# Performance work log

Measured on AMD Instinct MI355X. Metric: run time of the kernel, lower is better.

## Reference

```python
import jax, jax.numpy as jnp
import numpy as np
from jax import lax

KSIZE = 7

def _grid():
    # torch.linspace(-7//2, 7//2, 7) == linspace(-4, 3, 7): asymmetric, step 7/6
    x = np.linspace(-4.0, 3.0, KSIZE, dtype=np.float32).reshape(-1, 1)
    y = x.T
    return x, y

def _gaussian_kernel(sigma):
    x, y = _grid()
    g = np.exp(-(x ** 2 + y ** 2) / (2.0 * sigma ** 2))
    g = g / g.sum()
    return g.reshape(1, 1, KSIZE, KSIZE).astype(np.float32)

def _log_kernel(sigma):
    x, y = _grid()
    r2 = x ** 2 + y ** 2
    log = (1.0 - r2 / (2.0 * sigma ** 2)) * np.exp(-r2 / (2.0 * sigma ** 2))
    log = log / np.abs(log).sum()
    return log.reshape(1, 1, KSIZE, KSIZE).astype(np.float32)

SOBEL_X = jnp.asarray([[-1, 0, 1], [-2, 0, 2], [-1, 0, 1]], dtype=jnp.float32).reshape(1, 1, 3, 3)
SOBEL_Y = jnp.asarray([[-1, -2, -1], [0, 0, 0], [1, 2, 1]], dtype=jnp.float32).reshape(1, 1, 3, 3)
POINT = jnp.asarray([[0, -1, 0], [-1, 4, -1], [0, -1, 0]], dtype=jnp.float32).reshape(1, 1, 3, 3)
STRUCT_FILTERS = [jnp.asarray(_gaussian_kernel(s)) for s in (0.5, 1.0, 2.0)]
SCALE_FILTERS = [jnp.asarray(_log_kernel(s)) for s in (1.0, 2.0, 4.0)]

def _conv(x, k, pad):
    # torch F.conv2d == cross-correlation, which lax conv also computes (no kernel flip)
    return lax.conv_general_dilated(
        x, k, window_strides=(1, 1),
        padding=[(pad, pad), (pad, pad)],
        dimension_numbers=("NCHW", "OIHW", "NCHW"))

def _mse(a, b):
    d = a - b
    return jnp.mean(d * d)

def _maxpool3(x):
    # torch max_pool2d pads with -inf
    return lax.reduce_window(
        x, -jnp.inf, lax.max,
        window_dimensions=(1, 1, 3, 3), window_strides=(1, 1, 1, 1),
        padding=[(0, 0), (0, 0), (1, 1), (1, 1)])

def setup_inputs() -> dict:
    key = jax.random.key(0)
    k1, k2 = jax.random.split(key)
    shape = (64, 1, 512, 512)
    return {
        "reconstruction": jax.random.normal(k1, shape, dtype=jnp.float32),
        "target": jax.random.normal(k2, shape, dtype=jnp.float32),
    }

def reference(reconstruction, target):
    # intensity-weighted reconstruction loss
    w = (target > target.mean()).astype(reconstruction.dtype) * 2.0 + 1.0
    recon_loss = _mse(reconstruction * w, target * w)

    # gradient (sobel) loss
    gradient_loss = (
        _mse(_conv(reconstruction, SOBEL_X, 1), _conv(target, SOBEL_X, 1)) +
        _mse(_conv(reconstruction, SOBEL_Y, 1), _conv(target, SOBEL_Y, 1)))

    # point-source (laplacian) loss
    point_loss = _mse(_conv(reconstruction, POINT, 1), _conv(target, POINT, 1))

    # multi-scale gaussian structure loss
    structure_loss = 0.0
    for f in STRUCT_FILTERS:
        structure_loss += _mse(_conv(reconstruction, f, KSIZE // 2), _conv(target, f, KSIZE // 2))

    # LoG blob-scale loss
    scale_loss = 0.0
    for f in SCALE_FILTERS:
        scale_loss += _mse(_conv(reconstruction, f, KSIZE // 2), _conv(target, f, KSIZE // 2))

    # peak preservation via 3x3 max pool + L1
    peak_loss = jnp.mean(jnp.abs(_maxpool3(reconstruction) - _maxpool3(target)))

    return (recon_loss + 2.0 * gradient_loss + 1.5 * point_loss +
            1.0 * structure_loss + 1.0 * scale_loss + 2.0 * peak_loss)
```

## Files before the change

kernel.cpp:

```cpp
#include <hip/hip_runtime.h>
#include <math.h>

#define IMG 512
#define IMG2 (IMG * IMG)
#define NPIX (64 * IMG2)
#define ZPB 16

__device__ float g_c[64];

typedef __fp16 h2_t __attribute__((ext_vector_type(2)));

__device__ __forceinline__ float rdfl(float x) {
    return __uint_as_float(__builtin_amdgcn_readfirstlane(__float_as_uint(x)));
}
__device__ __forceinline__ unsigned int rdflu(float x) {
    return __builtin_amdgcn_readfirstlane(__float_as_uint(x));
}
__device__ __forceinline__ unsigned int as_u(h2_t h) {
    union { h2_t h; unsigned int u; } c;
    c.h = h;
    return c.u;
}
__device__ __forceinline__ h2_t as_h2(unsigned int u) {
    union { unsigned int u; h2_t h; } c;
    c.u = u;
    return c.h;
}
__device__ __forceinline__ h2_t h2z() {
    h2_t z = {(__fp16)0.f, (__fp16)0.f};
    return z;
}

__global__ void precompute_kernel() {
    if (threadIdx.x != 0 || blockIdx.x != 0) return;
    const double step = 7.0 / 6.0;
    float x[7];
    for (int j = 0; j < 7; j++) x[j] = (float)(-4.0 + j * step);
    x[6] = 3.0f;
    const float sigs[4] = {0.5f, 1.0f, 2.0f, 4.0f};
    float E[4][7], Q[4][7], Vv[3][7];
    for (int s = 0; s < 4; s++) {
        float inv = 1.0f / (2.0f * sigs[s] * sigs[s]);
        for (int j = 0; j < 7; j++) {
            float q = x[j] * x[j] * inv;
            Q[s][j] = q;
            E[s][j] = expf(-q);
        }
    }
    for (int s = 0; s < 3; s++)
        for (int j = 0; j < 7; j++) Vv[s][j] = Q[s + 1][j] * E[s + 1][j];

    auto pk2 = [](float a, float b) -> float {
        h2_t h;
        h[0] = (__fp16)a;
        h[1] = (__fp16)b;
        union { h2_t h; float f; } c;
        c.h = h;
        return c.f;
    };
    for (int k = 0; k < 7; k++) {
        g_c[k] = pk2(E[0][k], E[1][k]);
        g_c[7 + k] = pk2(E[2][k], E[3][k]);
        g_c[14 + k] = pk2(Vv[0][k], Vv[1][k]);
        g_c[21 + k] = pk2(Vv[2][k], Vv[2][k]);
        g_c[28 + k] = pk2(E[1][k], E[2][k]);
        g_c[35 + k] = pk2(E[2][k], -Vv[2][k]);
        g_c[42 + k] = pk2(-Vv[0][k], -Vv[1][k]);
        g_c[49 + k] = pk2(E[3][k], 0.f);
    }
    for (int s = 0; s < 3; s++) {
        float gs = 0.f;
        for (int i = 0; i < 7; i++)
            for (int j = 0; j < 7; j++) gs += E[s][i] * E[s][j];
        g_c[56 + s] = 1.0f / (gs * gs);
    }
    for (int s = 1; s < 4; s++) {
        float n = 0.f;
        for (int i = 0; i < 7; i++)
            for (int j = 0; j < 7; j++) {
                float v = E[s][i] * E[s][j] * (1.0f - Q[s][i] - Q[s][j]);
                n += fabsf(v);
            }
        g_c[59 + (s - 1)] = 1.0f / (n * n);
    }
    g_c[62] = 0.f;
    g_c[63] = 0.f;
}

__global__ __launch_bounds__(256) void sum_target_kernel(const float4* __restrict__ t4) {
    int tid = blockIdx.x * 256 + threadIdx.x;
    float s = 0.f;
    for (int i = tid; i < NPIX / 4; i += 2048 * 256) {
        float4 v = t4[i];
        s += (v.x + v.y) + (v.z + v.w);
    }
    for (int off = 32; off > 0; off >>= 1) s += __shfl_down(s, off);
    __shared__ float ps[4];
    int lane = threadIdx.x & 63, wid = threadIdx.x >> 6;
    if (lane == 0) ps[wid] = s;
    __syncthreads();
    if (threadIdx.x == 0) atomicAdd(&g_c[63], (ps[0] + ps[1]) + (ps[2] + ps[3]));
}

__global__ __launch_bounds__(256, 4) void main_kernel(const float* __restrict__ R,
                                                      const float* __restrict__ T) {
    __shared__ float sd[38][44];
    __shared__ float sr[34][40];
    __shared__ float st[34][40];
    __shared__ uint4 hrec[32][39];
    __shared__ float red[4];

    const int tid = threadIdx.x;
    const int gx0 = blockIdx.x * 32, gy0 = blockIdx.y * 32;
    const int z0 = blockIdx.z * ZPB;

    h2_t cE01[7], cE23[7], cV01[7], cV2[7], d2c[7], d3c[7], d4c[7], d5c[7];
#pragma unroll
    for (int k = 0; k < 7; k++) {
        cE01[k] = as_h2(rdflu(g_c[k]));
        cE23[k] = as_h2(rdflu(g_c[7 + k]));
        cV01[k] = as_h2(rdflu(g_c[14 + k]));
        cV2[k] = as_h2(rdflu(g_c[21 + k]));
        d2c[k] = as_h2(rdflu(g_c[28 + k]));
        d3c[k] = as_h2(rdflu(g_c[35 + k]));
        d4c[k] = as_h2(rdflu(g_c[42 + k]));
        d5c[k] = as_h2(rdflu(g_c[49 + k]));
    }
    float invS4[3], invN2[3];
#pragma unroll
    for (int s = 0; s < 3; s++) {
        invS4[s] = rdfl(g_c[56 + s]);
        invN2[s] = rdfl(g_c[59 + s]);
    }
    const float mean = rdfl(g_c[63]) * (1.0f / (float)NPIX);

    const int q0 = tid, q1 = tid + 256;
    const bool has1 = (q1 < 380);
    const int i0 = q0 / 10, c0 = q0 - 10 * i0;
    const int i1 = q1 / 10, c1 = q1 - 10 * i1;
    const int gy_0 = gy0 + i0 - 3, gxb0 = gx0 - 4 + 4 * c0;
    const int gy_1 = gy0 + i1 - 3, gxb1 = gx0 - 4 + 4 * c1;
    const int o0 = min(max(gy_0, 0), IMG - 1) * IMG + min(max(gxb0, 0), IMG - 4);
    const int o1 = min(max(gy_1, 0), IMG - 1) * IMG + min(max(gxb1, 0), IMG - 4);
    const bool vy0 = ((unsigned)gy_0 < IMG), vy1 = ((unsigned)gy_1 < IMG);
    bool m0[4], m1[4];
#pragma unroll
    for (int e = 0; e < 4; e++) {
        m0[e] = vy0 && ((unsigned)(gxb0 + e) < IMG);
        m1[e] = vy1 && ((unsigned)(gxb1 + e) < IMG);
    }

    const int x = tid & 31;
    const int y0 = (tid >> 5) * 4;

    float4 ra, ta, rb, tb;

#define LOAD_TILE(zz)                          \
    {                                          \
        const float* Rz = R + (long)(zz)*IMG2; \
        const float* Tz = T + (long)(zz)*IMG2; \
        ra = *(const float4*)(Rz + o0);        \
        ta = *(const float4*)(Tz + o0);        \
        if (has1) {                            \
            rb = *(const float4*)(Rz + o1);    \
            tb = *(const float4*)(Tz + o1);    \
        }                                      \
    }

#define WRITE_TILE()                                                                         \
    {                                                                                        \
        float rv[4] = {ra.x, ra.y, ra.z, ra.w};                                              \
        float tv[4] = {ta.x, ta.y, ta.z, ta.w};                                              \
        float dq[4], rq[4], tq[4];                                                           \
        _Pragma("unroll") for (int e = 0; e < 4; e++) {                                      \
            dq[e] = m0[e] ? (rv[e] - tv[e]) : 0.f;                                           \
            rq[e] = m0[e] ? rv[e] : -INFINITY;                                               \
            tq[e] = m0[e] ? tv[e] : -INFINITY;                                               \
        }                                                                                    \
        *(float4*)&sd[i0][4 * c0] = make_float4(dq[0], dq[1], dq[2], dq[3]);                 \
        if (i0 >= 2 && i0 < 36) {                                                            \
            *(float4*)&sr[i0 - 2][4 * c0] = make_float4(rq[0], rq[1], rq[2], rq[3]);         \
            *(float4*)&st[i0 - 2][4 * c0] = make_float4(tq[0], tq[1], tq[2], tq[3]);         \
        }                                                                                    \
        if (has1) {                                                                          \
            float rv1[4] = {rb.x, rb.y, rb.z, rb.w};                                         \
            float tv1[4] = {tb.x, tb.y, tb.z, tb.w};                                         \
            float dq1[4], rq1[4], tq1[4];                                                    \
            _Pragma("unroll") for (int e = 0; e < 4; e++) {                                  \
                dq1[e] = m1[e] ? (rv1[e] - tv1[e]) : 0.f;                                    \
                rq1[e] = m1[e] ? rv1[e] : -INFINITY;                                         \
                tq1[e] = m1[e] ? tv1[e] : -INFINITY;                                         \
            }                                                                                \
            *(float4*)&sd[i1][4 * c1] = make_float4(dq1[0], dq1[1], dq1[2], dq1[3]);         \
            if (i1 >= 2 && i1 < 36) {                                                        \
                *(float4*)&sr[i1 - 2][4 * c1] = make_float4(rq1[0], rq1[1], rq1[2], rq1[3]); \
                *(float4*)&st[i1 - 2][4 * c1] = make_float4(tq1[0], tq1[1], tq1[2], tq1[3]); \
            }                                                                                \
        }                                                                                    \
    }

    LOAD_TILE(z0);
    WRITE_TILE();
    __syncthreads();

    float total = 0.f;

    for (int it = 0; it < ZPB; ++it) {
        const bool havenext = (it + 1 < ZPB);
        if (havenext) LOAD_TILE(z0 + it + 1);

        {
            float dw[6][3];
#pragma unroll
            for (int r = 0; r < 6; r++)
#pragma unroll
                for (int c = 0; c < 3; c++) dw[r][c] = sd[y0 + 2 + r][x + 3 + c];
            float rx[6], rs[6];
#pragma unroll
            for (int r = 0; r < 6; r++) {
                rx[r] = dw[r][2] - dw[r][0];
                rs[r] = dw[r][0] + 2.f * dw[r][1] + dw[r][2];
            }
            float crm[6], ctm[6], tc[6];
#pragma unroll
            for (int r = 0; r < 6; r++) {
                float a = sr[y0 + r][x + 3], b = sr[y0 + r][x + 4], c = sr[y0 + r][x + 5];
                crm[r] = fmaxf(fmaxf(a, b), c);
                float a2 = st[y0 + r][x + 3], b2 = st[y0 + r][x + 4], c2 = st[y0 + r][x + 5];
                ctm[r] = fmaxf(fmaxf(a2, b2), c2);
                tc[r] = b2;
            }
#pragma unroll
            for (int yy = 0; yy < 4; yy++) {
                float sx = rx[yy] + 2.f * rx[yy + 1] + rx[yy + 2];
                float sy = rs[yy + 2] - rs[yy];
                float pt = 4.f * dw[yy + 1][1] - dw[yy][1] - dw[yy + 2][1] - dw[yy + 1][0] -
                           dw[yy + 1][2];
                float d = dw[yy + 1][1];
                float w2 = (tc[yy + 1] > mean) ? 9.f : 1.f;
                float mr = fmaxf(fmaxf(crm[yy], crm[yy + 1]), crm[yy + 2]);
                float mt = fmaxf(fmaxf(ctm[yy], ctm[yy + 1]), ctm[yy + 2]);
                total += w2 * d * d + 2.f * (sx * sx + sy * sy) + 1.5f * pt * pt +
                         2.f * fabsf(mr - mt);
            }
        }

        for (int j = tid; j < 304; j += 256) {
            int xq = j / 38, y = j - 38 * xq;
            const float* rp = &sd[y][4 * xq];
            float4 A = *(const float4*)(rp);
            float4 B = *(const float4*)(rp + 4);
            float4 C = *(const float4*)(rp + 8);
            float w[12] = {A.x, A.y, A.z, A.w, B.x, B.y, B.z, B.w, C.x, C.y, C.z, C.w};
            h2_t wp[12];
#pragma unroll
            for (int i = 0; i < 12; i++) wp[i] = __builtin_amdgcn_cvt_pkrtz(w[i], w[i]);
#pragma unroll
            for (int p = 0; p < 4; p++) {
                h2_t aE01 = h2z(), aE23 = h2z(), aV01 = h2z(), aV2 = h2z();
#pragma unroll
                for (int k = 0; k < 7; k++) {
                    h2_t d = wp[p + 1 + k];
                    aE01 = cE01[k] * d + aE01;
                    aE23 = cE23[k] * d + aE23;
                    aV01 = cV01[k] * d + aV01;
                    aV2 = cV2[k] * d + aV2;
                }
                h2_t he12 = __builtin_shufflevector(aE01, aE23, 1, 2);
                h2_t tm01 = he12 - aV01;
                h2_t he33 = __builtin_shufflevector(aE23, aE23, 1, 1);
                h2_t tm22 = he33 - aV2;
                hrec[4 * xq + p][y] =
                    make_uint4(as_u(aE01), as_u(aE23), as_u(tm01), as_u(tm22));
            }
        }
        __syncthreads();

        if (havenext) WRITE_TILE();

        {
            h2_t A1[4], A2[4], A3[4], A4[4], A5[4];
#pragma unroll
            for (int yy = 0; yy < 4; yy++) {
                A1[yy] = h2z();
                A2[yy] = h2z();
                A3[yy] = h2z();
                A4[yy] = h2z();
                A5[yy] = h2z();
            }
#pragma unroll
            for (int q = 0; q < 10; q++) {
                uint4 rec = hrec[x][y0 + q];
                h2_t rx = as_h2(rec.x), ry = as_h2(rec.y);
                h2_t rz = as_h2(rec.z), rw = as_h2(rec.w);
                h2_t r12 = __builtin_shufflevector(rx, ry, 1, 2);
#pragma unroll
                for (int yy = 0; yy < 4; yy++) {
                    const int k = q - yy;
                    if (k >= 0 && k <= 6) {
                        A1[yy] = cE01[k] * rx + A1[yy];
                        A2[yy] = d2c[k] * rz + A2[yy];
                        A3[yy] = d3c[k] * ry + A3[yy];
                        A4[yy] = d4c[k] * r12 + A4[yy];
                        A5[yy] = d5c[k] * rw + A5[yy];
                    }
                }
            }
#pragma unroll
            for (int yy = 0; yy < 4; yy++) {
                h2_t Bp = A2[yy] + A4[yy];
                float g0 = (float)A1[yy][0], g1 = (float)A1[yy][1];
                float g2 = (float)A3[yy][0];
                float aL0 = (float)Bp[0], aL1 = (float)Bp[1];
                float aL2 = (float)A5[yy][0] + (float)A3[yy][1];
                total += invS4[0] * g0 * g0 + invS4[1] * g1 * g1 + invS4[2] * g2 * g2 +
                         invN2[0] * aL0 * aL0 + invN2[1] * aL1 * aL1 + invN2[2] * aL2 * aL2;
            }
        }
        __syncthreads();
    }

    for (int off = 32; off > 0; off >>= 1) total += __shfl_down(total, off);
    int lane = tid & 63, wid = tid >> 6;
    if (lane == 0) red[wid] = total;
    __syncthreads();
    if (tid == 0) atomicAdd(&g_c[62], (red[0] + red[1]) + (red[2] + red[3]));
}

__global__ void finalize_kernel(float* __restrict__ out) {
    if (threadIdx.x == 0 && blockIdx.x == 0) out[0] = g_c[62] * (1.0f / (float)NPIX);
}

extern "C" void kernel_launch(void* const* d_in, const int* in_sizes, int n_in,
                              void* d_out, int out_size, void* d_ws, size_t ws_size,
                              hipStream_t stream) {
    const float* recon = (const float*)d_in[0];
    const float* target = (const float*)d_in[1];

    hipLaunchKernelGGL(precompute_kernel, dim3(1), dim3(64), 0, stream);
    hipLaunchKernelGGL(sum_target_kernel, dim3(2048), dim3(256), 0, stream,
                       (const float4*)target);
    dim3 grid(16, 16, 64 / ZPB), block(256);
    hipLaunchKernelGGL(main_kernel, grid, block, 0, stream, recon, target);
    hipLaunchKernelGGL(finalize_kernel, dim3(1), dim3(1), 0, stream, (float*)d_out);
}
```

Before: 130.0 us.

## Pack max-pool tiles to fp16 pairs, vectorize stencil loads, remove atomics

```diff
diff --git a/kernel.cpp b/kernel.cpp
--- a/kernel.cpp
+++ b/kernel.cpp
@@ -30,9 +30,11 @@
     h2_t z = {(__fp16)0.f, (__fp16)0.f};
     return z;
 }
-
-__global__ void precompute_kernel() {
-    if (threadIdx.x != 0 || blockIdx.x != 0) return;
+__device__ __forceinline__ h2_t hmax2(h2_t a, h2_t b) {
+    return __builtin_elementwise_max(a, b);
+}
+
+__device__ void compute_coeffs() {
     const double step = 7.0 / 6.0;
     float x[7];
     for (int j = 0; j < 7; j++) x[j] = (float)(-4.0 + j * step);
@@ -83,14 +85,13 @@
             }
         g_c[59 + (s - 1)] = 1.0f / (n * n);
     }
-    g_c[62] = 0.f;
-    g_c[63] = 0.f;
-}
-
-__global__ __launch_bounds__(256) void sum_target_kernel(const float4* __restrict__ t4) {
-    int tid = blockIdx.x * 256 + threadIdx.x;
+}
+
+__global__ __launch_bounds__(256) void sum_target_kernel(const float4* __restrict__ t4,
+                                                          float* __restrict__ ws) {
+    if (blockIdx.x == 0 && threadIdx.x == 0) compute_coeffs();
     float s = 0.f;
-    for (int i = tid; i < NPIX / 4; i += 2048 * 256) {
+    for (int i = blockIdx.x * 256 + threadIdx.x; i < NPIX / 4; i += 256 * 256) {
         float4 v = t4[i];
         s += (v.x + v.y) + (v.z + v.w);
     }
@@ -99,20 +100,30 @@
     int lane = threadIdx.x & 63, wid = threadIdx.x >> 6;
     if (lane == 0) ps[wid] = s;
     __syncthreads();
-    if (threadIdx.x == 0) atomicAdd(&g_c[63], (ps[0] + ps[1]) + (ps[2] + ps[3]));
+    if (threadIdx.x == 0) ws[blockIdx.x] = (ps[0] + ps[1]) + (ps[2] + ps[3]);
 }
 
 __global__ __launch_bounds__(256, 4) void main_kernel(const float* __restrict__ R,
-                                                      const float* __restrict__ T) {
+                                                      const float* __restrict__ T,
+                                                      float* __restrict__ ws) {
     __shared__ float sd[38][44];
-    __shared__ float sr[34][40];
-    __shared__ float st[34][40];
+    __shared__ unsigned srt[34][44];
     __shared__ uint4 hrec[32][39];
     __shared__ float red[4];
 
     const int tid = threadIdx.x;
     const int gx0 = blockIdx.x * 32, gy0 = blockIdx.y * 32;
     const int z0 = blockIdx.z * ZPB;
+    const int bid = blockIdx.x + (blockIdx.y << 4) + (blockIdx.z << 8);
+
+    {
+        float v = ws[tid];
+        for (int off = 32; off > 0; off >>= 1) v += __shfl_down(v, off);
+        int lane = tid & 63, wid = tid >> 6;
+        if (lane == 0) red[wid] = v;
+        __syncthreads();
+    }
+    const float mean = rdfl(((red[0] + red[1]) + (red[2] + red[3])) * (1.0f / (float)NPIX));
 
     h2_t cE01[7], cE23[7], cV01[7], cV2[7], d2c[7], d3c[7], d4c[7], d5c[7];
 #pragma unroll
@@ -132,7 +143,6 @@
         invS4[s] = rdfl(g_c[56 + s]);
         invN2[s] = rdfl(g_c[59 + s]);
     }
-    const float mean = rdfl(g_c[63]) * (1.0f / (float)NPIX);
 
     const int q0 = tid, q1 = tid + 256;
     const bool has1 = (q1 < 380);
@@ -152,6 +162,8 @@
 
     const int x = tid & 31;
     const int y0 = (tid >> 5) * 4;
+    const int py = tid >> 3;
+    const int cb = (tid & 7) * 4;
 
     float4 ra, ta, rb, tb;
 
@@ -167,36 +179,35 @@
         }                                      \
     }
 
-#define WRITE_TILE()                                                                         \
-    {                                                                                        \
-        float rv[4] = {ra.x, ra.y, ra.z, ra.w};                                              \
-        float tv[4] = {ta.x, ta.y, ta.z, ta.w};                                              \
-        float dq[4], rq[4], tq[4];                                                           \
-        _Pragma("unroll") for (int e = 0; e < 4; e++) {                                      \
-            dq[e] = m0[e] ? (rv[e] - tv[e]) : 0.f;                                           \
-            rq[e] = m0[e] ? rv[e] : -INFINITY;                                               \
-            tq[e] = m0[e] ? tv[e] : -INFINITY;                                               \
-        }                                                                                    \
-        *(float4*)&sd[i0][4 * c0] = make_float4(dq[0], dq[1], dq[2], dq[3]);                 \
-        if (i0 >= 2 && i0 < 36) {                                                            \
-            *(float4*)&sr[i0 - 2][4 * c0] = make_float4(rq[0], rq[1], rq[2], rq[3]);         \
-            *(float4*)&st[i0 - 2][4 * c0] = make_float4(tq[0], tq[1], tq[2], tq[3]);         \
-        }                                                                                    \
-        if (has1) {                                                                          \
-            float rv1[4] = {rb.x, rb.y, rb.z, rb.w};                                         \
-            float tv1[4] = {tb.x, tb.y, tb.z, tb.w};                                         \
-            float dq1[4], rq1[4], tq1[4];                                                    \
-            _Pragma("unroll") for (int e = 0; e < 4; e++) {                                  \
-                dq1[e] = m1[e] ? (rv1[e] - tv1[e]) : 0.f;                                    \
-                rq1[e] = m1[e] ? rv1[e] : -INFINITY;                                         \
-                tq1[e] = m1[e] ? tv1[e] : -INFINITY;                                         \
-            }                                                                                \
-            *(float4*)&sd[i1][4 * c1] = make_float4(dq1[0], dq1[1], dq1[2], dq1[3]);         \
-            if (i1 >= 2 && i1 < 36) {                                                        \
-                *(float4*)&sr[i1 - 2][4 * c1] = make_float4(rq1[0], rq1[1], rq1[2], rq1[3]); \
-                *(float4*)&st[i1 - 2][4 * c1] = make_float4(tq1[0], tq1[1], tq1[2], tq1[3]); \
-            }                                                                                \
-        }                                                                                    \
+#define WRITE_TILE()                                                                 \
+    {                                                                                \
+        float rv[4] = {ra.x, ra.y, ra.z, ra.w};                                      \
+        float tv[4] = {ta.x, ta.y, ta.z, ta.w};                                      \
+        float dq[4];                                                                 \
+        unsigned pkq[4];                                                             \
+        _Pragma("unroll") for (int e = 0; e < 4; e++) {                              \
+            dq[e] = m0[e] ? (rv[e] - tv[e]) : 0.f;                                   \
+            h2_t h = __builtin_amdgcn_cvt_pkrtz(rv[e], tv[e]);                       \
+            pkq[e] = m0[e] ? as_u(h) : 0xFC00FC00u;                                  \
+        }                                                                            \
+        *(float4*)&sd[i0][4 * c0] = make_float4(dq[0], dq[1], dq[2], dq[3]);         \
+        if (i0 >= 2 && i0 < 36)                                                      \
+            *(uint4*)&srt[i0 - 2][4 * c0] = make_uint4(pkq[0], pkq[1], pkq[2], pkq[3]); \
+        if (has1) {                                                                  \
+            float rv1[4] = {rb.x, rb.y, rb.z, rb.w};                                 \
+            float tv1[4] = {tb.x, tb.y, tb.z, tb.w};                                 \
+            float dq1[4];                                                            \
+            unsigned pkq1[4];                                                        \
+            _Pragma("unroll") for (int e = 0; e < 4; e++) {                          \
+                dq1[e] = m1[e] ? (rv1[e] - tv1[e]) : 0.f;                            \
+                h2_t h = __builtin_amdgcn_cvt_pkrtz(rv1[e], tv1[e]);                 \
+                pkq1[e] = m1[e] ? as_u(h) : 0xFC00FC00u;                             \
+            }                                                                        \
+            *(float4*)&sd[i1][4 * c1] = make_float4(dq1[0], dq1[1], dq1[2], dq1[3]); \
+            if (i1 >= 2 && i1 < 36)                                                  \
+                *(uint4*)&srt[i1 - 2][4 * c1] =                                      \
+                    make_uint4(pkq1[0], pkq1[1], pkq1[2], pkq1[3]);                  \
+        }                                                                            \
     }
 
     LOAD_TILE(z0);
@@ -210,36 +221,58 @@
         if (havenext) LOAD_TILE(z0 + it + 1);
 
         {
-            float dw[6][3];
-#pragma unroll
-            for (int r = 0; r < 6; r++)
-#pragma unroll
-                for (int c = 0; c < 3; c++) dw[r][c] = sd[y0 + 2 + r][x + 3 + c];
-            float rx[6], rs[6];
-#pragma unroll
-            for (int r = 0; r < 6; r++) {
-                rx[r] = dw[r][2] - dw[r][0];
-                rs[r] = dw[r][0] + 2.f * dw[r][1] + dw[r][2];
-            }
-            float crm[6], ctm[6], tc[6];
-#pragma unroll
-            for (int r = 0; r < 6; r++) {
-                float a = sr[y0 + r][x + 3], b = sr[y0 + r][x + 4], c = sr[y0 + r][x + 5];
-                crm[r] = fmaxf(fmaxf(a, b), c);
-                float a2 = st[y0 + r][x + 3], b2 = st[y0 + r][x + 4], c2 = st[y0 + r][x + 5];
-                ctm[r] = fmaxf(fmaxf(a2, b2), c2);
-                tc[r] = b2;
-            }
-#pragma unroll
-            for (int yy = 0; yy < 4; yy++) {
-                float sx = rx[yy] + 2.f * rx[yy + 1] + rx[yy + 2];
-                float sy = rs[yy + 2] - rs[yy];
-                float pt = 4.f * dw[yy + 1][1] - dw[yy][1] - dw[yy + 2][1] - dw[yy + 1][0] -
-                           dw[yy + 1][2];
-                float d = dw[yy + 1][1];
-                float w2 = (tc[yy + 1] > mean) ? 9.f : 1.f;
-                float mr = fmaxf(fmaxf(crm[yy], crm[yy + 1]), crm[yy + 2]);
-                float mt = fmaxf(fmaxf(ctm[yy], ctm[yy + 1]), ctm[yy + 2]);
+            float a0[8], a1[8], a2[8];
+            {
+                const float* p0 = &sd[py + 2][cb + 2];
+                const float* p1 = &sd[py + 3][cb + 2];
+                const float* p2 = &sd[py + 4][cb + 2];
+                float2 u;
+                float4 w;
+                u = *(const float2*)p0;       a0[0] = u.x; a0[1] = u.y;
+                w = *(const float4*)(p0 + 2); a0[2] = w.x; a0[3] = w.y; a0[4] = w.z; a0[5] = w.w;
+                u = *(const float2*)(p0 + 6); a0[6] = u.x; a0[7] = u.y;
+                u = *(const float2*)p1;       a1[0] = u.x; a1[1] = u.y;
+                w = *(const float4*)(p1 + 2); a1[2] = w.x; a1[3] = w.y; a1[4] = w.z; a1[5] = w.w;
+                u = *(const float2*)(p1 + 6); a1[6] = u.x; a1[7] = u.y;
+                u = *(const float2*)p2;       a2[0] = u.x; a2[1] = u.y;
+                w = *(const float4*)(p2 + 2); a2[2] = w.x; a2[3] = w.y; a2[4] = w.z; a2[5] = w.w;
+                u = *(const float2*)(p2 + 6); a2[6] = u.x; a2[7] = u.y;
+            }
+            unsigned uu0[6], uu1[6], uu2[6];
+            {
+                const unsigned* q0p = &srt[py][cb + 3];
+                const unsigned* q1p = &srt[py + 1][cb + 3];
+                const unsigned* q2p = &srt[py + 2][cb + 3];
+                uint4 m;
+                uu0[0] = q0p[0];
+                m = *(const uint4*)(q0p + 1);
+                uu0[1] = m.x; uu0[2] = m.y; uu0[3] = m.z; uu0[4] = m.w;
+                uu0[5] = q0p[5];
+                uu1[0] = q1p[0];
+                m = *(const uint4*)(q1p + 1);
+                uu1[1] = m.x; uu1[2] = m.y; uu1[3] = m.z; uu1[4] = m.w;
+                uu1[5] = q1p[5];
+                uu2[0] = q2p[0];
+                m = *(const uint4*)(q2p + 1);
+                uu2[1] = m.x; uu2[2] = m.y; uu2[3] = m.z; uu2[4] = m.w;
+                uu2[5] = q2p[5];
+            }
+            h2_t cm[6];
+#pragma unroll
+            for (int m = 0; m < 6; m++)
+                cm[m] = hmax2(hmax2(as_h2(uu0[m]), as_h2(uu1[m])), as_h2(uu2[m]));
+#pragma unroll
+            for (int e = 0; e < 4; e++) {
+                float sx = (a0[e + 3] - a0[e + 1]) + 2.f * (a1[e + 3] - a1[e + 1]) +
+                           (a2[e + 3] - a2[e + 1]);
+                float sy = (a2[e + 1] - a0[e + 1]) + 2.f * (a2[e + 2] - a0[e + 2]) +
+                           (a2[e + 3] - a0[e + 3]);
+                float pt = 4.f * a1[e + 2] - a0[e + 2] - a2[e + 2] - a1[e + 1] - a1[e + 3];
+                float d = a1[e + 2];
+                h2_t wm = hmax2(hmax2(cm[e], cm[e + 1]), cm[e + 2]);
+                float mr = (float)wm[0], mt = (float)wm[1];
+                float tc = (float)as_h2(uu1[e + 1])[1];
+                float w2 = (tc > mean) ? 9.f : 1.f;
                 total += w2 * d * d + 2.f * (sx * sx + sy * sy) + 1.5f * pt * pt +
                          2.f * fabsf(mr - mt);
             }
@@ -324,11 +357,20 @@
     int lane = tid & 63, wid = tid >> 6;
     if (lane == 0) red[wid] = total;
     __syncthreads();
-    if (tid == 0) atomicAdd(&g_c[62], (red[0] + red[1]) + (red[2] + red[3]));
-}
-
-__global__ void finalize_kernel(float* __restrict__ out) {
-    if (threadIdx.x == 0 && blockIdx.x == 0) out[0] = g_c[62] * (1.0f / (float)NPIX);
+    if (tid == 0) ws[256 + bid] = (red[0] + red[1]) + (red[2] + red[3]);
+}
+
+__global__ __launch_bounds__(256) void finalize_kernel(const float* __restrict__ ws,
+                                                       float* __restrict__ out) {
+    float s = 0.f;
+    for (int i = threadIdx.x; i < 1024; i += 256) s += ws[256 + i];
+    for (int off = 32; off > 0; off >>= 1) s += __shfl_down(s, off);
+    __shared__ float ps[4];
+    int lane = threadIdx.x & 63, wid = threadIdx.x >> 6;
+    if (lane == 0) ps[wid] = s;
+    __syncthreads();
+    if (threadIdx.x == 0)
+        out[0] = ((ps[0] + ps[1]) + (ps[2] + ps[3])) * (1.0f / (float)NPIX);
 }
 
 extern "C" void kernel_launch(void* const* d_in, const int* in_sizes, int n_in,
@@ -336,11 +378,11 @@
                               hipStream_t stream) {
     const float* recon = (const float*)d_in[0];
     const float* target = (const float*)d_in[1];
-
-    hipLaunchKernelGGL(precompute_kernel, dim3(1), dim3(64), 0, stream);
-    hipLaunchKernelGGL(sum_target_kernel, dim3(2048), dim3(256), 0, stream,
-                       (const float4*)target);
+    float* ws = (float*)d_ws;
+
+    hipLaunchKernelGGL(sum_target_kernel, dim3(256), dim3(256), 0, stream,
+                       (const float4*)target, ws);
     dim3 grid(16, 16, 64 / ZPB), block(256);
-    hipLaunchKernelGGL(main_kernel, grid, block, 0, stream, recon, target);
-    hipLaunchKernelGGL(finalize_kernel, dim3(1), dim3(1), 0, stream, (float*)d_out);
-}
+    hipLaunchKernelGGL(main_kernel, grid, block, 0, stream, recon, target, ws);
+    hipLaunchKernelGGL(finalize_kernel, dim3(1), dim3(256), 0, stream, ws, (float*)d_out);
+}
```

After: 133.2 us. 2.4% more time.
